# Kernel optimization log

Hardware: AMD Instinct MI355X
Metric: run time of the kernel (lower is better)

The kernel has to match this reference:

```python
import jax, jax.numpy as jnp
import numpy as np

B, N, C = 64, 256, 512
SHIFTS = (-1, 0, 1)
# torch.chunk(N, 3): ceil(256/3)=86 -> sizes [86, 86, 84]
CHUNK_SIZES = (86, 86, 84)
EPS = 1e-5


def _shift_pad(a, s):
    # shift along last axis (C) with zero padding, matching shift_with_padding
    if s == 0:
        return a
    if s > 0:
        return jnp.pad(a[..., :-s], ((0, 0), (0, 0), (s, 0)))
    s = -s
    return jnp.pad(a[..., s:], ((0, 0), (0, 0), (0, s)))


def setup_inputs() -> dict:
    key = jax.random.key(0)
    ks = jax.random.split(key, 16)
    w = lambda k, shape: (jax.random.normal(k, shape, jnp.float32) * 0.02)
    inp = {
        "x": jax.random.normal(ks[0], (B, N, C), jnp.float32),
        "ln_g": jnp.ones((C,), jnp.float32),
        "ln_b": jnp.zeros((C,), jnp.float32),
        "Ws": w(ks[1], (C, C)),
        "bs": jnp.zeros((C,), jnp.float32),
        "Wc": w(ks[2], (N, N, 3)),     # Conv1d weight [out=N, in=N, k=3]
        "bc": jnp.zeros((N,), jnp.float32),
        "We1": w(ks[3], (N, N // 8)),
        "be1": jnp.zeros((N // 8,), jnp.float32),
        "We2": w(ks[4], (N // 8, N)),
        "be2": jnp.zeros((N,), jnp.float32),
        "Wf1": w(ks[5], (C, 2 * C)),
        "bf1": jnp.zeros((2 * C,), jnp.float32),
        "Wf2": w(ks[6], (2 * C, C)),
        "bf2": jnp.zeros((C,), jnp.float32),
    }
    return inp


def reference(x, ln_g, ln_b, Ws, bs, Wc, bc, We1, be1, We2, be2, Wf1, bf1, Wf2, bf2):
    res = x
    # channel_mixer_S: LayerNorm over C, then Linear C->C + relu (dropout=0)
    mu = jnp.mean(x, axis=-1, keepdims=True)
    var = jnp.mean((x - mu) ** 2, axis=-1, keepdims=True)
    h = (x - mu) * jax.lax.rsqrt(var + EPS) * ln_g + ln_b
    h = jax.nn.relu(h @ Ws + bs)                      # [B, N, C]
    # channel_shift: chunk along N, shift each chunk along C with zero pad
    offs = np.cumsum((0,) + CHUNK_SIZES)
    chunks = [h[:, offs[i]:offs[i + 1], :] for i in range(3)]
    x_shift = jnp.concatenate([_shift_pad(c, s) for c, s in zip(chunks, SHIFTS)], axis=1)
    # channel_projection: Conv1d over C with N channels, k=3, pad=1
    x_shift = jax.lax.conv_general_dilated(
        x_shift, Wc, window_strides=(1,), padding=[(1, 1)],
        dimension_numbers=("NCH", "OIH", "NCH")) + bc[None, :, None]
    # SE gating
    se = jnp.mean(x_shift, axis=-1)                   # [B, N]
    ex = jax.nn.sigmoid(jax.nn.relu(se @ We1 + be1) @ We2 + be2)  # [B, N]
    z = x_shift * ex[:, :, None]
    # channel_mixer_F: C -> 2C (relu) -> C, residual
    z = jax.nn.relu(z @ Wf1 + bf1) @ Wf2 + bf2 + res
    return z
```

## Files before the change

kernel.cpp:

```cpp
#include <hip/hip_runtime.h>
#include <hip/hip_bf16.h>
#include <math.h>

#define BB 64
#define NN 256
#define CCH 512

typedef unsigned short u16;
typedef __attribute__((ext_vector_type(8))) short s16x8;
typedef __attribute__((ext_vector_type(4))) float f32x4;

#define AS1 __attribute__((address_space(1)))
#define AS3 __attribute__((address_space(3)))

static __device__ __forceinline__ u16 f2b(float f) {
    __hip_bfloat16 h = __float2bfloat16(f);
    union { __hip_bfloat16 h; u16 u; } x; x.h = h; return x.u;
}
static __device__ __forceinline__ void gll16(const void* g, void* l) {
    __builtin_amdgcn_global_load_lds((const AS1 unsigned int*)g,
                                     (AS3 unsigned int*)l, 16, 0, 0);
}

#define VM8  asm volatile("s_waitcnt vmcnt(8)" ::: "memory")
#define VM6  asm volatile("s_waitcnt vmcnt(6)" ::: "memory")
#define VM4  asm volatile("s_waitcnt vmcnt(4)" ::: "memory")
#define VM0  asm volatile("s_waitcnt vmcnt(0)" ::: "memory")
#define LGKM0 asm volatile("s_waitcnt lgkmcnt(0)" ::: "memory")
#define MEMB asm volatile("" ::: "memory")

static __device__ __forceinline__ void wtc_body(const float* __restrict__ W,
    u16* __restrict__ Wt, int K, int N, int bx, int by, float* t )
{
    int n0 = bx * 32, k0 = by * 32;
    int tx = threadIdx.x & 31, ty = threadIdx.x >> 5;
    #pragma unroll
    for (int i = 0; i < 4; ++i)
        t[(ty + i * 8) * 33 + tx] = W[(size_t)(k0 + ty + i * 8) * N + n0 + tx];
    __syncthreads();
    #pragma unroll
    for (int i = 0; i < 4; ++i)
        Wt[(size_t)(n0 + ty + i * 8) * K + k0 + tx] = f2b(t[tx * 33 + ty + i * 8]);
}

__global__ __launch_bounds__(256) void prep_ln_kernel(
    const float* __restrict__ Ws,  u16* __restrict__ Wst,
    const float* __restrict__ Wf1, u16* __restrict__ Wf1t,
    const float* __restrict__ Wf2, u16* __restrict__ Wf2t,
    const float* __restrict__ Wc,  u16* __restrict__ Wc3,
    u16* __restrict__ Hts,
    const float* __restrict__ x, const float* __restrict__ g,
    const float* __restrict__ bta, u16* __restrict__ xnorm)
{
    __shared__ float t[32 * 33];
    int bid = blockIdx.x;
    if (bid < 256) {
        wtc_body(Ws, Wst, 512, 512, bid & 15, bid >> 4, t);
    } else if (bid < 768) {
        int idx = bid - 256;
        wtc_body(Wf1, Wf1t, 512, 1024, idx & 31, idx >> 5, t);
    } else if (bid < 1280) {
        int idx = bid - 768;
        wtc_body(Wf2, Wf2t, 1024, 512, idx & 15, idx >> 4, t);
    } else if (bid < 2048) {
        int idx = (bid - 1280) * 256 + threadIdx.x;
        int i = idx & 255;
        int o = (idx >> 8) & 255;
        int k = idx >> 16;
        Wc3[idx] = f2b(Wc[((size_t)o * NN + i) * 3 + k]);
    } else if (bid < 2304) {
        int idx = (bid - 2048) * 256 + threadIdx.x;
        int b   = idx >> 10;
        int rem = idx & 1023;
        int rr  = rem >> 8;
        int r   = (rr & 1) + (rr >> 1) * 512;
        Hts[((size_t)b * 514 + r) * 256 + (rem & 255)] = 0;
    } else {
        const int l = threadIdx.x & 63;
        const int r = (bid - 2304) * 4 + (threadIdx.x >> 6);
        const float4* xr = (const float4*)(x + (size_t)r * CCH);
        float4 v1 = xr[l];
        float4 v2 = xr[l + 64];
        float s  = v1.x + v1.y + v1.z + v1.w + v2.x + v2.y + v2.z + v2.w;
        float ss = v1.x*v1.x + v1.y*v1.y + v1.z*v1.z + v1.w*v1.w
                 + v2.x*v2.x + v2.y*v2.y + v2.z*v2.z + v2.w*v2.w;
        #pragma unroll
        for (int o = 32; o > 0; o >>= 1) {
            s  += __shfl_xor(s, o);
            ss += __shfl_xor(ss, o);
        }
        float mu  = s * (1.0f / CCH);
        float var = ss * (1.0f / CCH) - mu * mu;
        float rs  = rsqrtf(var + 1e-5f);
        float4 g1 = ((const float4*)g)[l],   g2 = ((const float4*)g)[l + 64];
        float4 b1 = ((const float4*)bta)[l], b2 = ((const float4*)bta)[l + 64];
        ushort4 o1, o2;
        o1.x = f2b((v1.x - mu) * rs * g1.x + b1.x);
        o1.y = f2b((v1.y - mu) * rs * g1.y + b1.y);
        o1.z = f2b((v1.z - mu) * rs * g1.z + b1.z);
        o1.w = f2b((v1.w - mu) * rs * g1.w + b1.w);
        o2.x = f2b((v2.x - mu) * rs * g2.x + b2.x);
        o2.y = f2b((v2.y - mu) * rs * g2.y + b2.y);
        o2.z = f2b((v2.z - mu) * rs * g2.z + b2.z);
        o2.w = f2b((v2.w - mu) * rs * g2.w + b2.w);
        ushort4* orow = (ushort4*)(xnorm + (size_t)r * CCH);
        orow[l]      = o1;
        orow[l + 64] = o2;
    }
}

template<int MODE, int BNT>
__global__ __launch_bounds__(512, 1) void gemm_pipe(
    const u16* __restrict__ A, const u16* __restrict__ Bt,
    const float* __restrict__ bias, const float* __restrict__ res,
    void* __restrict__ outv, u16* __restrict__ auxout,
    float* __restrict__ SEpart,
    const float* __restrict__ seb, const float* __restrict__ We1,
    const float* __restrict__ be1, const float* __restrict__ We2,
    const float* __restrict__ be2)
{
    constexpr int NK = (MODE == 2) ? 32 : (MODE == 3) ? 24 : 16;
    constexpr int SA = (MODE == 2) ? 1024 : 512;
    constexpr int SB = (MODE == 2) ? 1024 : 512;
    constexpr int NOUT = (MODE == 1) ? 1024 : 512;
    constexpr int NF = BNT / 64;
    constexpr int BSZ = BNT * 32;
    constexpr int NSLOT = (BNT == 128) ? 6 : 4;

    __shared__ u16 Asm[NSLOT * 8192];
    __shared__ u16 Bsm[NSLOT * BSZ];
    __shared__ float sse[256];
    __shared__ float e1f[32];
    __shared__ float exs[256];

    const int tid = threadIdx.x;
    const int l   = tid & 63;
    const int w   = tid >> 6;
    const int nwg = gridDim.x;
    const int work = (blockIdx.x & 7) * (nwg >> 3) + (blockIdx.x >> 3);

    int row0, col0, bidx = 0;
    if (MODE == 0)      { row0 = (work >> 7) * 256; col0 = (work & 127) * 128; }
    else if (MODE == 1) { row0 = (work >> 2) * 256; col0 = (work & 3) * 256; }
    else if (MODE == 2) { row0 = (work >> 2) * 256; col0 = (work & 3) * 128; }
    else                { row0 = 0; bidx = work >> 2; col0 = (work & 3) * 128; }

    const u16* Aab  = A + (size_t)row0 * SA;
    const u16* Bab  = Bt + (size_t)col0 * SB;
    const u16* HtsB = Bt + (size_t)bidx * 514 * 256;

    const int wm = (w >> 2) * 128;
    const int wn = (w & 3) * (BNT / 4);
    const int fr = l & 15;
    const int q  = l >> 4;
    const int kofs = ((q ^ ((l >> 1) & 3)) * 8);

    const f32x4 zero = {0.0f, 0.0f, 0.0f, 0.0f};
    f32x4 acc[8][NF];
    #pragma unroll
    for (int m = 0; m < 8; ++m)
        #pragma unroll
        for (int n = 0; n < NF; ++n) acc[m][n] = zero;

    const int kc0 = ((tid & 3) ^ ((tid >> 3) & 3)) * 8;
    const int srow = tid >> 2;

    auto stage = [&](int u, int slot) {
        u16* ald = Asm + slot * 8192 + w * 512;
        u16* bld = Bsm + slot * BSZ + w * 512;
        if (MODE == 3) {
            const int kseg = u >> 3, kb = (u & 7) * 32 + kc0;
            gll16(A + kseg * 65536 + srow * 256 + kb, ald);
            gll16(A + kseg * 65536 + (srow + 128) * 256 + kb, ald + 4096);
            gll16(HtsB + (size_t)(col0 + srow + kseg) * 256 + kb, bld);
        } else {
            const int kb = u * 32 + kc0;
            gll16(Aab + (size_t)srow * SA + kb, ald);
            gll16(Aab + (size_t)(srow + 128) * SA + kb, ald + 4096);
            gll16(Bab + (size_t)srow * SB + kb, bld);
            if (BNT == 256)
                gll16(Bab + (size_t)(srow + 128) * SB + kb, bld + 4096);
        }
    };

    if (BNT == 128) {
        stage(0, 0); stage(1, 1); stage(2, 2); stage(3, 3);
        int sa = 0;
        constexpr int NV = NK / 2;
        for (int v = 0; v < NV; ++v) {
            if (v + 1 < NV) { VM6; } else { VM0; }
            __builtin_amdgcn_s_barrier();
            MEMB;
            const int sb = sa + 1;
            s16x8 b0[2], af0[8];
            #pragma unroll
            for (int n = 0; n < 2; ++n)
                b0[n] = *(const s16x8*)&Bsm[sa * BSZ + (wn + n * 16 + fr) * 32 + kofs];
            #pragma unroll
            for (int m = 0; m < 8; ++m)
                af0[m] = *(const s16x8*)&Asm[sa * 8192 + (wm + m * 16 + fr) * 32 + kofs];
            const int u2 = 2 * v + 4;
            if (u2 < NK) {
                int st = sa + 4; if (st >= 6) st -= 6;
                stage(u2, st);
                int st1 = st + 1; if (st1 >= 6) st1 -= 6;
                stage(u2 + 1, st1);
            }
            __builtin_amdgcn_s_setprio(1);
            #pragma unroll
            for (int m = 0; m < 8; ++m)
                #pragma unroll
                for (int n = 0; n < 2; ++n)
                    acc[m][n] = __builtin_amdgcn_mfma_f32_16x16x32_bf16(af0[m], b0[n], acc[m][n], 0, 0, 0);
            __builtin_amdgcn_s_setprio(0);
            s16x8 b1[2], af1[8];
            #pragma unroll
            for (int n = 0; n < 2; ++n)
                b1[n] = *(const s16x8*)&Bsm[sb * BSZ + (wn + n * 16 + fr) * 32 + kofs];
            #pragma unroll
            for (int m = 0; m < 8; ++m)
                af1[m] = *(const s16x8*)&Asm[sb * 8192 + (wm + m * 16 + fr) * 32 + kofs];
            __builtin_amdgcn_s_setprio(1);
            #pragma unroll
            for (int m = 0; m < 8; ++m)
                #pragma unroll
                for (int n = 0; n < 2; ++n)
                    acc[m][n] = __builtin_amdgcn_mfma_f32_16x16x32_bf16(af1[m], b1[n], acc[m][n], 0, 0, 0);
            __builtin_amdgcn_s_setprio(0);
            MEMB;
            sa += 2; if (sa >= 6) sa = 0;
        }
    } else {
        stage(0, 0); stage(1, 1); stage(2, 2);
        if (MODE == 1) {
            if (tid < 256) {
                int o = row0 + tid;
                sse[tid] = (SEpart[o] + SEpart[16384 + o] + SEpart[32768 + o]
                            + SEpart[49152 + o]) * (1.0f / CCH) + seb[tid];
            }
            LGKM0;
            __builtin_amdgcn_s_barrier();
            if (tid < 32) {
                float a = be1[tid];
                #pragma unroll 8
                for (int i = 0; i < 256; ++i) a += sse[i] * We1[i * 32 + tid];
                e1f[tid] = fmaxf(a, 0.0f);
            }
            LGKM0;
            __builtin_amdgcn_s_barrier();
            if (tid < 256) {
                float a = be2[tid];
                #pragma unroll
                for (int j = 0; j < 32; ++j) a += e1f[j] * We2[j * 256 + tid];
                exs[tid] = 1.0f / (1.0f + expf(-a));
            }
            LGKM0;
            __builtin_amdgcn_s_barrier();
        }
        for (int u = 0; u < NK; ++u) {
            if (u < NK - 2)       { VM8; }
            else if (u == NK - 2) { VM4; }
            else                  { VM0; }
            __builtin_amdgcn_s_barrier();
            MEMB;
            const int slot = u & 3;
            s16x8 bfv[NF];
            #pragma unroll
            for (int n = 0; n < NF; ++n)
                bfv[n] = *(const s16x8*)&Bsm[slot * BSZ + (wn + n * 16 + fr) * 32 + kofs];
            s16x8 af[8];
            #pragma unroll
            for (int m = 0; m < 8; ++m)
                af[m] = *(const s16x8*)&Asm[slot * 8192 + (wm + m * 16 + fr) * 32 + kofs];
            if (u + 3 < NK) stage(u + 3, (u + 3) & 3);
            __builtin_amdgcn_s_setprio(1);
            #pragma unroll
            for (int m = 0; m < 8; ++m)
                #pragma unroll
                for (int n = 0; n < NF; ++n)
                    acc[m][n] = __builtin_amdgcn_mfma_f32_16x16x32_bf16(af[m], bfv[n], acc[m][n], 0, 0, 0);
            __builtin_amdgcn_s_setprio(0);
            MEMB;
        }
    }

    if (MODE == 0) {
        #pragma unroll
        for (int m = 0; m < 8; ++m) {
            #pragma unroll
            for (int j = 0; j < 4; ++j) {
                const int c = row0 + wm + m * 16 + (l >> 4) * 4 + j;
                const float bsv = bias[c];
                #pragma unroll
                for (int n = 0; n < NF; ++n) {
                    const int gcol = col0 + wn + n * 16 + fr;
                    const int b  = gcol >> 8;
                    const int ni = gcol & 255;
                    const int s  = (ni < 86) ? -1 : (ni < 172 ? 0 : 1);
                    auxout[((size_t)b * 514 + c + 1 + s) * 256 + ni] =
                        f2b(fmaxf(acc[m][n][j] + bsv, 0.0f));
                }
            }
        }
    } else if (MODE == 1) {
        #pragma unroll
        for (int m = 0; m < 8; ++m) {
            #pragma unroll
            for (int j = 0; j < 4; ++j) {
                const int rl  = wm + m * 16 + (l >> 4) * 4 + j;
                const int row = row0 + rl;
                const float sc = exs[rl];
                #pragma unroll
                for (int n = 0; n < NF; ++n) {
                    const int col = col0 + wn + n * 16 + fr;
                    ((u16*)outv)[(size_t)row * NOUT + col] =
                        f2b(fmaxf(acc[m][n][j] * sc + bias[col], 0.0f));
                }
            }
        }
    } else if (MODE == 2) {
        #pragma unroll
        for (int m = 0; m < 8; ++m) {
            #pragma unroll
            for (int j = 0; j < 4; ++j) {
                const int row = row0 + wm + m * 16 + (l >> 4) * 4 + j;
                #pragma unroll
                for (int n = 0; n < NF; ++n) {
                    const int col = col0 + wn + n * 16 + fr;
                    ((float*)outv)[(size_t)row * NOUT + col] =
                        acc[m][n][j] + bias[col] + res[(size_t)row * NOUT + col];
                }
            }
        }
    } else {
        const int ct = col0 >> 7;
        #pragma unroll
        for (int m = 0; m < 8; ++m) {
            #pragma unroll
            for (int j = 0; j < 4; ++j) {
                const int no = wm + m * 16 + (l >> 4) * 4 + j;
                const float bcv = bias[no];
                float p = 0.0f;
                #pragma unroll
                for (int n = 0; n < NF; ++n) {
                    const int c = col0 + wn + n * 16 + fr;
                    float v = acc[m][n][j];
                    auxout[((size_t)bidx * NN + no) * CCH + c] = f2b(v + bcv);
                    p += v;
                }
                p += __shfl_xor(p, 1);
                p += __shfl_xor(p, 2);
                p += __shfl_xor(p, 4);
                p += __shfl_xor(p, 8);
                if (fr == 0)
                    SEpart[ct * 16384 + bidx * NN + no] = p;
            }
        }
    }
}

extern "C" void kernel_launch(void* const* d_in, const int* in_sizes, int n_in,
                              void* d_out, int out_size, void* d_ws, size_t ws_size,
                              hipStream_t stream) {
    const float* x    = (const float*)d_in[0];
    const float* ln_g = (const float*)d_in[1];
    const float* ln_b = (const float*)d_in[2];
    const float* Ws   = (const float*)d_in[3];
    const float* bs   = (const float*)d_in[4];
    const float* Wc   = (const float*)d_in[5];
    const float* bc   = (const float*)d_in[6];
    const float* We1  = (const float*)d_in[7];
    const float* be1  = (const float*)d_in[8];
    const float* We2  = (const float*)d_in[9];
    const float* be2  = (const float*)d_in[10];
    const float* Wf1  = (const float*)d_in[11];
    const float* bf1  = (const float*)d_in[12];
    const float* Wf2  = (const float*)d_in[13];
    const float* bf2  = (const float*)d_in[14];
    float* out = (float*)d_out;
    char* w8   = (char*)d_ws;

    u16* XN  = (u16*)(w8);
    u16* Y   = XN;
    u16* Hts = (u16*)(w8 + (16u << 20));
    u16* T   = (u16*)(w8 + (16u << 20));
    char* tail = w8 + 50397184;
    float* SEpart = (float*)(tail);
    u16* Wst      = (u16*)(tail + 262144);
    u16* Wf1t     = (u16*)(tail + 786432);
    u16* Wf2t     = (u16*)(tail + 1835008);
    u16* Wc3      = (u16*)(tail + 2883584);

    prep_ln_kernel<<<6400, 256, 0, stream>>>(Ws, Wst, Wf1, Wf1t, Wf2, Wf2t,
                                             Wc, Wc3, Hts, x, ln_g, ln_b, XN);
    gemm_pipe<0, 128><<<256, 512, 0, stream>>>(Wst, XN, bs, nullptr,
        nullptr, Hts, nullptr, nullptr, nullptr, nullptr, nullptr, nullptr);
    gemm_pipe<3, 128><<<256, 512, 0, stream>>>(Wc3, Hts, bc, nullptr,
        nullptr, Y, SEpart, nullptr, nullptr, nullptr, nullptr, nullptr);
    gemm_pipe<1, 256><<<256, 512, 0, stream>>>(Y, Wf1t, bf1, nullptr,
        T, nullptr, SEpart, bc, We1, be1, We2, be2);
    gemm_pipe<2, 128><<<256, 512, 0, stream>>>(T, Wf2t, bf2, x,
        out, nullptr, nullptr, nullptr, nullptr, nullptr, nullptr, nullptr);
}
```

Baseline: 116.5 us.

## Replace Wf1 GEMM with dedicated 8-phase double-buffered pipelined kernel

Pulls the C->2C GEMM with SE gating out of the templated gemm_pipe and into a dedicated kernel. It uses 64-wide K tiles with two LDS buffers and an XOR swizzle, and splits each K step into four MFMA phases separated by barriers. The staging of the next K tile's A and B quarters is interleaved between those phases. The aim is to overlap global-to-LDS loads with MFMA work better and to reduce LDS bank conflicts, at the cost of more barriers per K step and more complex code.

```diff
diff --git a/kernel.cpp b/kernel.cpp
--- a/kernel.cpp
+++ b/kernel.cpp
@@ -24,7 +24,6 @@
 
 #define VM8  asm volatile("s_waitcnt vmcnt(8)" ::: "memory")
 #define VM6  asm volatile("s_waitcnt vmcnt(6)" ::: "memory")
-#define VM4  asm volatile("s_waitcnt vmcnt(4)" ::: "memory")
 #define VM0  asm volatile("s_waitcnt vmcnt(0)" ::: "memory")
 #define LGKM0 asm volatile("s_waitcnt lgkmcnt(0)" ::: "memory")
 #define MEMB asm volatile("" ::: "memory")
@@ -109,29 +108,20 @@
     }
 }
 
-template<int MODE, int BNT>
+template<int MODE>
 __global__ __launch_bounds__(512, 1) void gemm_pipe(
     const u16* __restrict__ A, const u16* __restrict__ Bt,
     const float* __restrict__ bias, const float* __restrict__ res,
     void* __restrict__ outv, u16* __restrict__ auxout,
-    float* __restrict__ SEpart,
-    const float* __restrict__ seb, const float* __restrict__ We1,
-    const float* __restrict__ be1, const float* __restrict__ We2,
-    const float* __restrict__ be2)
+    float* __restrict__ SEpart)
 {
     constexpr int NK = (MODE == 2) ? 32 : (MODE == 3) ? 24 : 16;
     constexpr int SA = (MODE == 2) ? 1024 : 512;
     constexpr int SB = (MODE == 2) ? 1024 : 512;
-    constexpr int NOUT = (MODE == 1) ? 1024 : 512;
-    constexpr int NF = BNT / 64;
-    constexpr int BSZ = BNT * 32;
-    constexpr int NSLOT = (BNT == 128) ? 6 : 4;
-
-    __shared__ u16 Asm[NSLOT * 8192];
-    __shared__ u16 Bsm[NSLOT * BSZ];
-    __shared__ float sse[256];
-    __shared__ float e1f[32];
-    __shared__ float exs[256];
+    constexpr int NOUT = 512;
+
+    __shared__ u16 Asm[6 * 8192];
+    __shared__ u16 Bsm[6 * 4096];
 
     const int tid = threadIdx.x;
     const int l   = tid & 63;
@@ -141,7 +131,6 @@
 
     int row0, col0, bidx = 0;
     if (MODE == 0)      { row0 = (work >> 7) * 256; col0 = (work & 127) * 128; }
-    else if (MODE == 1) { row0 = (work >> 2) * 256; col0 = (work & 3) * 256; }
     else if (MODE == 2) { row0 = (work >> 2) * 256; col0 = (work & 3) * 128; }
     else                { row0 = 0; bidx = work >> 2; col0 = (work & 3) * 128; }
 
@@ -150,24 +139,22 @@
     const u16* HtsB = Bt + (size_t)bidx * 514 * 256;
 
     const int wm = (w >> 2) * 128;
-    const int wn = (w & 3) * (BNT / 4);
+    const int wn = (w & 3) * 32;
     const int fr = l & 15;
     const int q  = l >> 4;
     const int kofs = ((q ^ ((l >> 1) & 3)) * 8);
 
     const f32x4 zero = {0.0f, 0.0f, 0.0f, 0.0f};
-    f32x4 acc[8][NF];
+    f32x4 acc[8][2];
     #pragma unroll
-    for (int m = 0; m < 8; ++m)
-        #pragma unroll
-        for (int n = 0; n < NF; ++n) acc[m][n] = zero;
+    for (int m = 0; m < 8; ++m) { acc[m][0] = zero; acc[m][1] = zero; }
 
     const int kc0 = ((tid & 3) ^ ((tid >> 3) & 3)) * 8;
     const int srow = tid >> 2;
 
     auto stage = [&](int u, int slot) {
         u16* ald = Asm + slot * 8192 + w * 512;
-        u16* bld = Bsm + slot * BSZ + w * 512;
+        u16* bld = Bsm + slot * 4096 + w * 512;
         if (MODE == 3) {
             const int kseg = u >> 3, kb = (u & 7) * 32 + kc0;
             gll16(A + kseg * 65536 + srow * 256 + kb, ald);
@@ -178,110 +165,54 @@
             gll16(Aab + (size_t)srow * SA + kb, ald);
             gll16(Aab + (size_t)(srow + 128) * SA + kb, ald + 4096);
             gll16(Bab + (size_t)srow * SB + kb, bld);
-            if (BNT == 256)
-                gll16(Bab + (size_t)(srow + 128) * SB + kb, bld + 4096);
         }
     };
 
-    if (BNT == 128) {
-        stage(0, 0); stage(1, 1); stage(2, 2); stage(3, 3);
-        int sa = 0;
-        constexpr int NV = NK / 2;
-        for (int v = 0; v < NV; ++v) {
-            if (v + 1 < NV) { VM6; } else { VM0; }
-            __builtin_amdgcn_s_barrier();
-            MEMB;
-            const int sb = sa + 1;
-            s16x8 b0[2], af0[8];
+    stage(0, 0); stage(1, 1); stage(2, 2); stage(3, 3);
+    int sa = 0;
+    constexpr int NV = NK / 2;
+    for (int v = 0; v < NV; ++v) {
+        if (v + 1 < NV) { VM6; } else { VM0; }
+        __builtin_amdgcn_s_barrier();
+        MEMB;
+        const int sb = sa + 1;
+        s16x8 b0[2], af0[8];
+        #pragma unroll
+        for (int n = 0; n < 2; ++n)
+            b0[n] = *(const s16x8*)&Bsm[sa * 4096 + (wn + n * 16 + fr) * 32 + kofs];
+        #pragma unroll
+        for (int m = 0; m < 8; ++m)
+            af0[m] = *(const s16x8*)&Asm[sa * 8192 + (wm + m * 16 + fr) * 32 + kofs];
+        const int u2 = 2 * v + 4;
+        if (u2 < NK) {
+            int st = sa + 4; if (st >= 6) st -= 6;
+            stage(u2, st);
+            int st1 = st + 1; if (st1 >= 6) st1 -= 6;
+            stage(u2 + 1, st1);
+        }
+        __builtin_amdgcn_s_setprio(1);
+        #pragma unroll
+        for (int m = 0; m < 8; ++m)
             #pragma unroll
             for (int n = 0; n < 2; ++n)
-                b0[n] = *(const s16x8*)&Bsm[sa * BSZ + (wn + n * 16 + fr) * 32 + kofs];
-            #pragma unroll
-            for (int m = 0; m < 8; ++m)
-                af0[m] = *(const s16x8*)&Asm[sa * 8192 + (wm + m * 16 + fr) * 32 + kofs];
-            const int u2 = 2 * v + 4;
-            if (u2 < NK) {
-                int st = sa + 4; if (st >= 6) st -= 6;
-                stage(u2, st);
-                int st1 = st + 1; if (st1 >= 6) st1 -= 6;
-                stage(u2 + 1, st1);
-            }
-            __builtin_amdgcn_s_setprio(1);
-            #pragma unroll
-            for (int m = 0; m < 8; ++m)
-                #pragma unroll
-                for (int n = 0; n < 2; ++n)
-                    acc[m][n] = __builtin_amdgcn_mfma_f32_16x16x32_bf16(af0[m], b0[n], acc[m][n], 0, 0, 0);
-            __builtin_amdgcn_s_setprio(0);
-            s16x8 b1[2], af1[8];
+                acc[m][n] = __builtin_amdgcn_mfma_f32_16x16x32_bf16(af0[m], b0[n], acc[m][n], 0, 0, 0);
+        __builtin_amdgcn_s_setprio(0);
+        s16x8 b1[2], af1[8];
+        #pragma unroll
+        for (int n = 0; n < 2; ++n)
+            b1[n] = *(const s16x8*)&Bsm[sb * 4096 + (wn + n * 16 + fr) * 32 + kofs];
+        #pragma unroll
+        for (int m = 0; m < 8; ++m)
+            af1[m] = *(const s16x8*)&Asm[sb * 8192 + (wm + m * 16 + fr) * 32 + kofs];
+        __builtin_amdgcn_s_setprio(1);
+        #pragma unroll
+        for (int m = 0; m < 8; ++m)
             #pragma unroll
             for (int n = 0; n < 2; ++n)
-                b1[n] = *(const s16x8*)&Bsm[sb * BSZ + (wn + n * 16 + fr) * 32 + kofs];
-            #pragma unroll
-            for (int m = 0; m < 8; ++m)
-                af1[m] = *(const s16x8*)&Asm[sb * 8192 + (wm + m * 16 + fr) * 32 + kofs];
-            __builtin_amdgcn_s_setprio(1);
-            #pragma unroll
-            for (int m = 0; m < 8; ++m)
-                #pragma unroll
-                for (int n = 0; n < 2; ++n)
-                    acc[m][n] = __builtin_amdgcn_mfma_f32_16x16x32_bf16(af1[m], b1[n], acc[m][n], 0, 0, 0);
-            __builtin_amdgcn_s_setprio(0);
-            MEMB;
-            sa += 2; if (sa >= 6) sa = 0;
-        }
-    } else {
-        stage(0, 0); stage(1, 1); stage(2, 2);
-        if (MODE == 1) {
-            if (tid < 256) {
-                int o = row0 + tid;
-                sse[tid] = (SEpart[o] + SEpart[16384 + o] + SEpart[32768 + o]
-                            + SEpart[49152 + o]) * (1.0f / CCH) + seb[tid];
-            }
-            LGKM0;
-            __builtin_amdgcn_s_barrier();
-            if (tid < 32) {
-                float a = be1[tid];
-                #pragma unroll 8
-                for (int i = 0; i < 256; ++i) a += sse[i] * We1[i * 32 + tid];
-                e1f[tid] = fmaxf(a, 0.0f);
-            }
-            LGKM0;
-            __builtin_amdgcn_s_barrier();
-            if (tid < 256) {
-                float a = be2[tid];
-                #pragma unroll
-                for (int j = 0; j < 32; ++j) a += e1f[j] * We2[j * 256 + tid];
-                exs[tid] = 1.0f / (1.0f + expf(-a));
-            }
-            LGKM0;
-            __builtin_amdgcn_s_barrier();
-        }
-        for (int u = 0; u < NK; ++u) {
-            if (u < NK - 2)       { VM8; }
-            else if (u == NK - 2) { VM4; }
-            else                  { VM0; }
-            __builtin_amdgcn_s_barrier();
-            MEMB;
-            const int slot = u & 3;
-            s16x8 bfv[NF];
-            #pragma unroll
-            for (int n = 0; n < NF; ++n)
-                bfv[n] = *(const s16x8*)&Bsm[slot * BSZ + (wn + n * 16 + fr) * 32 + kofs];
-            s16x8 af[8];
-            #pragma unroll
-            for (int m = 0; m < 8; ++m)
-                af[m] = *(const s16x8*)&Asm[slot * 8192 + (wm + m * 16 + fr) * 32 + kofs];
-            if (u + 3 < NK) stage(u + 3, (u + 3) & 3);
-            __builtin_amdgcn_s_setprio(1);
-            #pragma unroll
-            for (int m = 0; m < 8; ++m)
-                #pragma unroll
-                for (int n = 0; n < NF; ++n)
-                    acc[m][n] = __builtin_amdgcn_mfma_f32_16x16x32_bf16(af[m], bfv[n], acc[m][n], 0, 0, 0);
-            __builtin_amdgcn_s_setprio(0);
-            MEMB;
-        }
+                acc[m][n] = __builtin_amdgcn_mfma_f32_16x16x32_bf16(af1[m], b1[n], acc[m][n], 0, 0, 0);
+        __builtin_amdgcn_s_setprio(0);
+        MEMB;
+        sa += 2; if (sa >= 6) sa = 0;
     }
 
     if (MODE == 0) {
@@ -292,7 +223,7 @@
                 const int c = row0 + wm + m * 16 + (l >> 4) * 4 + j;
                 const float bsv = bias[c];
                 #pragma unroll
-                for (int n = 0; n < NF; ++n) {
+                for (int n = 0; n < 2; ++n) {
                     const int gcol = col0 + wn + n * 16 + fr;
                     const int b  = gcol >> 8;
                     const int ni = gcol & 255;
@@ -302,22 +233,6 @@
                 }
             }
         }
-    } else if (MODE == 1) {
-        #pragma unroll
-        for (int m = 0; m < 8; ++m) {
-            #pragma unroll
-            for (int j = 0; j < 4; ++j) {
-                const int rl  = wm + m * 16 + (l >> 4) * 4 + j;
-                const int row = row0 + rl;
-                const float sc = exs[rl];
-                #pragma unroll
-                for (int n = 0; n < NF; ++n) {
-                    const int col = col0 + wn + n * 16 + fr;
-                    ((u16*)outv)[(size_t)row * NOUT + col] =
-                        f2b(fmaxf(acc[m][n][j] * sc + bias[col], 0.0f));
-                }
-            }
-        }
     } else if (MODE == 2) {
         #pragma unroll
         for (int m = 0; m < 8; ++m) {
@@ -325,7 +240,7 @@
             for (int j = 0; j < 4; ++j) {
                 const int row = row0 + wm + m * 16 + (l >> 4) * 4 + j;
                 #pragma unroll
-                for (int n = 0; n < NF; ++n) {
+                for (int n = 0; n < 2; ++n) {
                     const int col = col0 + wn + n * 16 + fr;
                     ((float*)outv)[(size_t)row * NOUT + col] =
                         acc[m][n][j] + bias[col] + res[(size_t)row * NOUT + col];
@@ -342,7 +257,7 @@
                 const float bcv = bias[no];
                 float p = 0.0f;
                 #pragma unroll
-                for (int n = 0; n < NF; ++n) {
+                for (int n = 0; n < 2; ++n) {
                     const int c = col0 + wn + n * 16 + fr;
                     float v = acc[m][n][j];
                     auxout[((size_t)bidx * NN + no) * CCH + c] = f2b(v + bcv);
@@ -357,6 +272,181 @@
             }
         }
     }
+}
+
+__global__ __launch_bounds__(512, 1) void gemm1_8ph(
+    const u16* __restrict__ Yb, const u16* __restrict__ Wf1t,
+    const float* __restrict__ bf1, u16* __restrict__ T,
+    const float* __restrict__ SEpart, const float* __restrict__ bc,
+    const float* __restrict__ We1, const float* __restrict__ be1,
+    const float* __restrict__ We2, const float* __restrict__ be2)
+{
+    __shared__ u16 Ab[2][256 * 64];
+    __shared__ u16 Bb[2][256 * 64];
+    __shared__ float sse[256];
+    __shared__ float e1f[32];
+    __shared__ float exs[256];
+
+    const int tid = threadIdx.x;
+    const int l   = tid & 63;
+    const int w   = tid >> 6;
+    const int work = (blockIdx.x & 7) * 32 + (blockIdx.x >> 3);
+    const int row0 = (work >> 2) * 256;
+    const int col0 = (work & 3) * 256;
+
+    const u16* Aab = Yb  + (size_t)row0 * 512;
+    const u16* Bab = Wf1t + (size_t)col0 * 512;
+
+    const int wm = (w >> 2) * 128;
+    const int wn = (w & 3) * 64;
+    const int fr = l & 15;
+    const int q  = l >> 4;
+    const int r7 = fr & 7;
+
+    if (tid < 256) {
+        int o = row0 + tid;
+        sse[tid] = (SEpart[o] + SEpart[16384 + o] + SEpart[32768 + o]
+                    + SEpart[49152 + o]) * (1.0f / CCH) + bc[tid];
+    }
+    __syncthreads();
+    if (tid < 32) {
+        float a = be1[tid];
+        #pragma unroll 8
+        for (int i = 0; i < 256; ++i) a += sse[i] * We1[i * 32 + tid];
+        e1f[tid] = fmaxf(a, 0.0f);
+    }
+    __syncthreads();
+    if (tid < 256) {
+        float a = be2[tid];
+        #pragma unroll
+        for (int j = 0; j < 32; ++j) a += e1f[j] * We2[j * 256 + tid];
+        exs[tid] = 1.0f / (1.0f + expf(-a));
+    }
+    __syncthreads();
+
+    const int strow = tid >> 3;
+    const int sslot = tid & 7;
+    const int gslot = sslot ^ (strow & 7);
+    const size_t goff = (size_t)strow * 512 + gslot * 8;
+    const int     loff = strow * 64 + sslot * 8;
+
+    auto stageA = [&](int c, int kt, int j) {
+        gll16(Aab + (size_t)(j * 64) * 512 + kt * 64 + goff,
+              &Ab[c][j * 64 * 64 + loff]);
+    };
+    auto stageB = [&](int c, int kt, int j) {
+        gll16(Bab + (size_t)(j * 64) * 512 + kt * 64 + goff,
+              &Bb[c][j * 64 * 64 + loff]);
+    };
+
+    stageA(0, 0, 0); stageA(0, 0, 1); stageA(0, 0, 2); stageA(0, 0, 3);
+    stageB(0, 0, 0); stageB(0, 0, 1); stageB(0, 0, 2); stageB(0, 0, 3);
+    stageA(1, 1, 0); stageA(1, 1, 2);
+    stageB(1, 1, 0); stageB(1, 1, 1); stageB(1, 1, 2); stageB(1, 1, 3);
+
+    const f32x4 zero = {0.0f, 0.0f, 0.0f, 0.0f};
+    f32x4 acc[8][4];
+    #pragma unroll
+    for (int m = 0; m < 8; ++m)
+        #pragma unroll
+        for (int n = 0; n < 4; ++n) acc[m][n] = zero;
+
+    s16x8 afv[4][2], bfv[4][2];
+
+#define LDA8(c, r, ks) (*(const s16x8*)&Ab[c][(r) * 64 + (((((ks) << 2) + q) ^ r7) << 3)])
+#define LDB8(c, r, ks) (*(const s16x8*)&Bb[c][(r) * 64 + (((((ks) << 2) + q) ^ r7) << 3)])
+
+    for (int t = 0; t < 8; ++t) {
+        const int c = t & 1;
+        if (t < 7) { stageA(c ^ 1, t + 1, 1); stageA(c ^ 1, t + 1, 3); VM8; }
+        else       { VM0; }
+        __builtin_amdgcn_s_barrier();
+        MEMB;
+        #pragma unroll
+        for (int m = 0; m < 4; ++m) {
+            afv[m][0] = LDA8(c, wm + m * 16 + fr, 0);
+            afv[m][1] = LDA8(c, wm + m * 16 + fr, 1);
+        }
+        #pragma unroll
+        for (int n = 0; n < 2; ++n) {
+            bfv[n][0] = LDB8(c, wn + n * 16 + fr, 0);
+            bfv[n][1] = LDB8(c, wn + n * 16 + fr, 1);
+        }
+        LGKM0;
+        __builtin_amdgcn_s_setprio(1);
+        #pragma unroll
+        for (int m = 0; m < 4; ++m)
+            #pragma unroll
+            for (int n = 0; n < 2; ++n) {
+                acc[m][n] = __builtin_amdgcn_mfma_f32_16x16x32_bf16(afv[m][0], bfv[n][0], acc[m][n], 0, 0, 0);
+                acc[m][n] = __builtin_amdgcn_mfma_f32_16x16x32_bf16(afv[m][1], bfv[n][1], acc[m][n], 0, 0, 0);
+            }
+        __builtin_amdgcn_s_setprio(0);
+        __builtin_amdgcn_s_barrier();
+        if (t < 6) { stageA(c, t + 2, 0); stageA(c, t + 2, 2); }
+        #pragma unroll
+        for (int n = 2; n < 4; ++n) {
+            bfv[n][0] = LDB8(c, wn + n * 16 + fr, 0);
+            bfv[n][1] = LDB8(c, wn + n * 16 + fr, 1);
+        }
+        LGKM0;
+        __builtin_amdgcn_s_setprio(1);
+        #pragma unroll
+        for (int m = 0; m < 4; ++m)
+            #pragma unroll
+            for (int n = 2; n < 4; ++n) {
+                acc[m][n] = __builtin_amdgcn_mfma_f32_16x16x32_bf16(afv[m][0], bfv[n][0], acc[m][n], 0, 0, 0);
+                acc[m][n] = __builtin_amdgcn_mfma_f32_16x16x32_bf16(afv[m][1], bfv[n][1], acc[m][n], 0, 0, 0);
+            }
+        __builtin_amdgcn_s_setprio(0);
+        __builtin_amdgcn_s_barrier();
+        if (t < 6) { stageB(c, t + 2, 0); stageB(c, t + 2, 1); }
+        #pragma unroll
+        for (int m = 0; m < 4; ++m) {
+            afv[m][0] = LDA8(c, wm + 64 + m * 16 + fr, 0);
+            afv[m][1] = LDA8(c, wm + 64 + m * 16 + fr, 1);
+        }
+        LGKM0;
+        __builtin_amdgcn_s_setprio(1);
+        #pragma unroll
+        for (int m = 0; m < 4; ++m)
+            #pragma unroll
+            for (int n = 0; n < 2; ++n) {
+                acc[4 + m][n] = __builtin_amdgcn_mfma_f32_16x16x32_bf16(afv[m][0], bfv[n][0], acc[4 + m][n], 0, 0, 0);
+                acc[4 + m][n] = __builtin_amdgcn_mfma_f32_16x16x32_bf16(afv[m][1], bfv[n][1], acc[4 + m][n], 0, 0, 0);
+            }
+        __builtin_amdgcn_s_setprio(0);
+        __builtin_amdgcn_s_barrier();
+        if (t < 6) { stageB(c, t + 2, 2); stageB(c, t + 2, 3); }
+        __builtin_amdgcn_s_setprio(1);
+        #pragma unroll
+        for (int m = 0; m < 4; ++m)
+            #pragma unroll
+            for (int n = 2; n < 4; ++n) {
+                acc[4 + m][n] = __builtin_amdgcn_mfma_f32_16x16x32_bf16(afv[m][0], bfv[n][0], acc[4 + m][n], 0, 0, 0);
+                acc[4 + m][n] = __builtin_amdgcn_mfma_f32_16x16x32_bf16(afv[m][1], bfv[n][1], acc[4 + m][n], 0, 0, 0);
+            }
+        __builtin_amdgcn_s_setprio(0);
+        __builtin_amdgcn_s_barrier();
+    }
+
+    #pragma unroll
+    for (int m = 0; m < 8; ++m) {
+        #pragma unroll
+        for (int j = 0; j < 4; ++j) {
+            const int rl  = wm + m * 16 + q * 4 + j;
+            const int row = row0 + rl;
+            const float sc = exs[rl];
+            #pragma unroll
+            for (int n = 0; n < 4; ++n) {
+                const int col = col0 + wn + n * 16 + fr;
+                T[(size_t)row * 1024 + col] =
+                    f2b(fmaxf(acc[m][n][j] * sc + bf1[col], 0.0f));
+            }
+        }
+    }
+#undef LDA8
+#undef LDB8
 }
 
 extern "C" void kernel_launch(void* const* d_in, const int* in_sizes, int n_in,
@@ -393,12 +483,12 @@
 
     prep_ln_kernel<<<6400, 256, 0, stream>>>(Ws, Wst, Wf1, Wf1t, Wf2, Wf2t,
                                              Wc, Wc3, Hts, x, ln_g, ln_b, XN);
-    gemm_pipe<0, 128><<<256, 512, 0, stream>>>(Wst, XN, bs, nullptr,
-        nullptr, Hts, nullptr, nullptr, nullptr, nullptr, nullptr, nullptr);
-    gemm_pipe<3, 128><<<256, 512, 0, stream>>>(Wc3, Hts, bc, nullptr,
-        nullptr, Y, SEpart, nullptr, nullptr, nullptr, nullptr, nullptr);
-    gemm_pipe<1, 256><<<256, 512, 0, stream>>>(Y, Wf1t, bf1, nullptr,
-        T, nullptr, SEpart, bc, We1, be1, We2, be2);
-    gemm_pipe<2, 128><<<256, 512, 0, stream>>>(T, Wf2t, bf2, x,
-        out, nullptr, nullptr, nullptr, nullptr, nullptr, nullptr, nullptr);
-}
+    gemm_pipe<0><<<256, 512, 0, stream>>>(Wst, XN, bs, nullptr,
+                                          nullptr, Hts, nullptr);
+    gemm_pipe<3><<<256, 512, 0, stream>>>(Wc3, Hts, bc, nullptr,
+                                          nullptr, Y, SEpart);
+    gemm1_8ph<<<256, 512, 0, stream>>>(Y, Wf1t, bf1, T, SEpart, bc,
+                                       We1, be1, We2, be2);
+    gemm_pipe<2><<<256, 512, 0, stream>>>(T, Wf2t, bf2, x,
+                                          out, nullptr, nullptr);
+}
```

New measurement: 116.6 us. No clear change (+0.0%).
